# Performance work log

Hardware: AMD Instinct MI355X
Metric: run time of the kernel (lower is better)

Reference implementation:

```python
import jax, jax.numpy as jnp
import numpy as np

B, N, A, D = 16, 256, 64, 256


def setup_inputs() -> dict:
    key = jax.random.key(0)
    ks = jax.random.split(key, 9)
    s = 1.0 / np.sqrt(D)
    return {
        "cc_embeds": jax.random.normal(ks[0], (B, N, D), jnp.float32),
        "anchor_embeds": jax.random.normal(ks[1], (B, N, A, D), jnp.float32),
        "sims": jax.random.normal(ks[2], (B, N, A), jnp.float32),
        "Wq": jax.random.normal(ks[3], (D, D), jnp.float32) * s,
        "bq": jax.random.normal(ks[4], (D,), jnp.float32) * s,
        "Wk": jax.random.normal(ks[5], (D, D), jnp.float32) * s,
        "bk": jax.random.normal(ks[6], (D,), jnp.float32) * s,
        "Wv": jax.random.normal(ks[7], (D, D), jnp.float32) * s,
        "bv": jax.random.normal(ks[8], (D,), jnp.float32) * s,
    }


def reference(cc_embeds, anchor_embeds, sims, Wq, bq, Wk, bk, Wv, bv):
    # Linear projections (torch nn.Linear: x @ W.T + b)
    Q = cc_embeds @ Wq.T + bq                    # [B, N, D]
    K = anchor_embeds @ Wk.T + bk                # [B, N, A, D]
    V = anchor_embeds @ Wv.T + bv                # [B, N, A, D]
    scale = 1.0 / jnp.sqrt(jnp.asarray(D, Q.dtype))
    scores = jnp.einsum('bnd,bnad->bna', Q, K) * scale  # [B, N, A]
    adj = scores + sims                          # additive similarity bias
    # conditional softmax: rows whose raw sum == 0 are passed through unchanged
    nonzero = jnp.sum(adj, axis=-1, keepdims=True) != 0
    probs = jnp.where(nonzero, jax.nn.softmax(adj, axis=-1), adj)
    out = jnp.einsum('bna,bnad->bnd', probs, V)  # [B, N, D]
    return out[:, :, None, :]                    # match torch output [B, N, 1, D]
```

## Files before the change

kernel.cpp:

```cpp
#include <hip/hip_runtime.h>
#include <hip/hip_bf16.h>


__global__ __launch_bounds__(256) void k1_prep(
    const float* __restrict__ Wq, const float* __restrict__ bq,
    const float* __restrict__ Wk, const float* __restrict__ bk,
    const float* __restrict__ Wv,
    float* __restrict__ M, float* __restrict__ rvec, float* __restrict__ uvec,
    float* __restrict__ s0, float* __restrict__ WvT) {
  __shared__ float colL[256];
  __shared__ float pr[256];
  __shared__ float tile[64][65];
  const int tid = threadIdx.x;
  const int bid = blockIdx.x;
  if (bid < 256) {
    colL[tid] = Wq[tid * 256 + bid];
    __syncthreads();
    float acc = 0.f;
#pragma unroll 4
    for (int d = 0; d < 256; ++d) acc += colL[d] * Wk[d * 256 + tid];
    M[bid * 256 + tid] = acc;
  } else if (bid == 256) {
    colL[tid] = bq[tid];
    __syncthreads();
    float acc = 0.f;
#pragma unroll 4
    for (int d = 0; d < 256; ++d) acc += colL[d] * Wk[d * 256 + tid];
    rvec[tid] = acc;
  } else if (bid == 257) {
    colL[tid] = bk[tid];
    pr[tid] = bq[tid] * bk[tid];
    __syncthreads();
    float acc = 0.f;
#pragma unroll 4
    for (int d = 0; d < 256; ++d) acc += Wq[d * 256 + tid] * colL[d];
    uvec[tid] = acc;
    if (tid == 0) {
      float s = 0.f;
      for (int d = 0; d < 256; ++d) s += pr[d];
      s0[0] = s;
    }
  } else {
    const int tb = bid - 258, bi = tb >> 2, bj = tb & 3;
#pragma unroll
    for (int k = 0; k < 16; ++k) {
      int idx = k * 256 + tid;
      int r = idx >> 6, cL = idx & 63;
      tile[r][cL] = Wv[(bi * 64 + r) * 256 + bj * 64 + cL];
    }
    __syncthreads();
#pragma unroll
    for (int k = 0; k < 16; ++k) {
      int idx = k * 256 + tid;
      int r = idx >> 6, cL = idx & 63;
      WvT[(bj * 64 + r) * 256 + bi * 64 + cL] = tile[cL][r];
    }
  }
}

__global__ __launch_bounds__(256) void k2_proj(
    const float* __restrict__ cc, const float* __restrict__ M,
    const float* __restrict__ rvec, const float* __restrict__ uvec,
    const float* __restrict__ s0p,
    float* __restrict__ tmat, float* __restrict__ cvec) {
  __shared__ __align__(16) float ccT[256 * 8];
  __shared__ float uL[256];
  const int tid = threadIdx.x;
  const int i0 = blockIdx.x * 8;
  const float4* g4 = (const float4*)(cc + (size_t)i0 * 256);
#pragma unroll
  for (int k = 0; k < 2; ++k) {
    int f = k * 256 + tid;
    float4 v = g4[f];
    int row = f >> 6;
    int e = (f & 63) << 2;
    ccT[(e + 0) * 8 + row] = v.x;
    ccT[(e + 1) * 8 + row] = v.y;
    ccT[(e + 2) * 8 + row] = v.z;
    ccT[(e + 3) * 8 + row] = v.w;
  }
  uL[tid] = uvec[tid];
  __syncthreads();
  float acc[8] = {0.f, 0.f, 0.f, 0.f, 0.f, 0.f, 0.f, 0.f};
#pragma unroll 4
  for (int e = 0; e < 256; ++e) {
    float m = M[e * 256 + tid];
    const float4* cr = (const float4*)(ccT + e * 8);
    float4 c0 = cr[0], c1 = cr[1];
    acc[0] += c0.x * m; acc[1] += c0.y * m; acc[2] += c0.z * m; acc[3] += c0.w * m;
    acc[4] += c1.x * m; acc[5] += c1.y * m; acc[6] += c1.z * m; acc[7] += c1.w * m;
  }
  float rv = rvec[tid];
#pragma unroll
  for (int r = 0; r < 8; ++r) tmat[(size_t)(i0 + r) * 256 + tid] = acc[r] + rv;
  const int r = tid >> 5, j = tid & 31;
  float pc = 0.f;
#pragma unroll
  for (int k = 0; k < 8; ++k) pc += ccT[(j + 32 * k) * 8 + r] * uL[j + 32 * k];
  for (int off = 16; off >= 1; off >>= 1) pc += __shfl_xor(pc, off, 32);
  if (j == 0) cvec[i0 + r] = pc + s0p[0];
}

__global__ __launch_bounds__(256) void k3_attn(
    const float* __restrict__ anchor, const float* __restrict__ sims,
    const float* __restrict__ tmat, const float* __restrict__ cvec,
    float* __restrict__ wout, float* __restrict__ psum) {
  __shared__ float sL[64];
  __shared__ float pL[64];
  __shared__ __align__(16) float pW[4 * 256];
  __shared__ float psh;
  const int i = blockIdx.x;
  const int tid = threadIdx.x;
  const int lane = tid & 63, w = tid >> 6;

  const float4* g4 = (const float4*)(anchor + (size_t)i * 16384);
  float4 v[16];
#pragma unroll
  for (int k = 0; k < 16; ++k) v[k] = g4[k * 256 + tid];
  const float4 t4 = ((const float4*)(tmat + (size_t)i * 256))[lane];

#pragma unroll
  for (int k = 0; k < 16; ++k) {
    float s = v[k].x * t4.x + v[k].y * t4.y + v[k].z * t4.z + v[k].w * t4.w;
#pragma unroll
    for (int off = 32; off >= 1; off >>= 1) s += __shfl_xor(s, off, 64);
    if (lane == 0) sL[k * 4 + w] = s;
  }
  __syncthreads();
  if (tid < 64) {
    float adj = (sL[tid] + cvec[i]) * 0.0625f + sims[(size_t)i * 64 + tid];
    float ssum = adj, smax = adj;
    for (int off = 32; off >= 1; off >>= 1) {
      ssum += __shfl_xor(ssum, off, 64);
      smax = fmaxf(smax, __shfl_xor(smax, off, 64));
    }
    float p;
    if (ssum != 0.f) {
      p = expf(adj - smax);
      float z = p;
      for (int off = 32; off >= 1; off >>= 1) z += __shfl_xor(z, off, 64);
      p = p / z;
    } else {
      p = adj;
    }
    float ps = p;
    for (int off = 32; off >= 1; off >>= 1) ps += __shfl_xor(ps, off, 64);
    pL[tid] = p;
    if (tid == 0) psh = ps;
  }
  __syncthreads();
  float4 acc = {0.f, 0.f, 0.f, 0.f};
#pragma unroll
  for (int k = 0; k < 16; ++k) {
    float p = pL[k * 4 + w];
    acc.x += p * v[k].x; acc.y += p * v[k].y;
    acc.z += p * v[k].z; acc.w += p * v[k].w;
  }
  ((float4*)(pW + w * 256))[lane] = acc;
  __syncthreads();
  float val = pW[tid] + pW[256 + tid] + pW[512 + tid] + pW[768 + tid];
  wout[(size_t)i * 256 + tid] = val;
  if (tid == 0) psum[i] = psh;
}

__global__ __launch_bounds__(256) void k4_out(
    const float* __restrict__ wmat, const float* __restrict__ WvT,
    const float* __restrict__ bv, const float* __restrict__ psum,
    float* __restrict__ out) {
  __shared__ __align__(16) float wT[256 * 8];
  __shared__ float psL[8];
  const int tid = threadIdx.x;
  const int i0 = blockIdx.x * 8;
  const float4* g4 = (const float4*)(wmat + (size_t)i0 * 256);
#pragma unroll
  for (int k = 0; k < 2; ++k) {
    int f = k * 256 + tid;
    float4 v = g4[f];
    int row = f >> 6;
    int e = (f & 63) << 2;
    wT[(e + 0) * 8 + row] = v.x;
    wT[(e + 1) * 8 + row] = v.y;
    wT[(e + 2) * 8 + row] = v.z;
    wT[(e + 3) * 8 + row] = v.w;
  }
  if (tid < 8) psL[tid] = psum[i0 + tid];
  __syncthreads();
  float acc[8] = {0.f, 0.f, 0.f, 0.f, 0.f, 0.f, 0.f, 0.f};
#pragma unroll 4
  for (int e = 0; e < 256; ++e) {
    float m = WvT[e * 256 + tid];
    const float4* wr = (const float4*)(wT + e * 8);
    float4 c0 = wr[0], c1 = wr[1];
    acc[0] += c0.x * m; acc[1] += c0.y * m; acc[2] += c0.z * m; acc[3] += c0.w * m;
    acc[4] += c1.x * m; acc[5] += c1.y * m; acc[6] += c1.z * m; acc[7] += c1.w * m;
  }
  float b = bv[tid];
#pragma unroll
  for (int r = 0; r < 8; ++r)
    out[(size_t)(i0 + r) * 256 + tid] = acc[r] + b * psL[r];
}

extern "C" void kernel_launch(void* const* d_in, const int* in_sizes, int n_in,
                              void* d_out, int out_size, void* d_ws, size_t ws_size,
                              hipStream_t stream) {
  const float* cc     = (const float*)d_in[0];
  const float* anchor = (const float*)d_in[1];
  const float* sims   = (const float*)d_in[2];
  const float* Wq     = (const float*)d_in[3];
  const float* bq     = (const float*)d_in[4];
  const float* Wk     = (const float*)d_in[5];
  const float* bk     = (const float*)d_in[6];
  const float* Wv     = (const float*)d_in[7];
  const float* bv     = (const float*)d_in[8];
  float* out = (float*)d_out;
  float* ws  = (float*)d_ws;

  float* M    = ws;
  float* WvT  = ws + 65536;
  float* rvec = ws + 131072;
  float* uvec = ws + 131328;
  float* s0   = ws + 131584;
  float* cvec = ws + 131840;
  float* psum = ws + 135936;
  float* tmat = ws + 140032;
  float* wmat = tmat + 1048576;

  k1_prep<<<274, 256, 0, stream>>>(Wq, bq, Wk, bk, Wv, M, rvec, uvec, s0, WvT);
  k2_proj<<<512, 256, 0, stream>>>(cc, M, rvec, uvec, s0, tmat, cvec);
  k3_attn<<<4096, 256, 0, stream>>>(anchor, sims, tmat, cvec, wmat, psum);
  k4_out<<<512, 256, 0, stream>>>(wmat, WvT, bv, psum, out);
}
```

Measured before the change: 461.0 us.

## Split-K projection GEMVs with readlane broadcast and nontemporal anchor loads

The small projection kernels (k2 and k4) now split the reduction dimension across the four wavefronts. Each lane holds one input element per row and broadcasts it with readlane, and each lane computes four output columns using vector loads of the weight matrix. The partial sums are combined through shared memory. The attention kernel loads the streamed anchor tensor with nontemporal loads so it does not pollute the cache. The cost is more shared memory and registers in the GEMV kernels, while the dominant streaming kernel is left mostly unchanged.

```diff
diff --git a/kernel.cpp b/kernel.cpp
--- a/kernel.cpp
+++ b/kernel.cpp
@@ -1,6 +1,12 @@
 #include <hip/hip_runtime.h>
 #include <hip/hip_bf16.h>
 
+
+typedef float f4 __attribute__((ext_vector_type(4)));
+
+__device__ __forceinline__ float bcast_lane(float x, int lane) {
+  return __int_as_float(__builtin_amdgcn_readlane(__float_as_int(x), lane));
+}
 
 __global__ __launch_bounds__(256) void k1_prep(
     const float* __restrict__ Wq, const float* __restrict__ bq,
@@ -63,42 +69,45 @@
     const float* __restrict__ rvec, const float* __restrict__ uvec,
     const float* __restrict__ s0p,
     float* __restrict__ tmat, float* __restrict__ cvec) {
-  __shared__ __align__(16) float ccT[256 * 8];
-  __shared__ float uL[256];
-  const int tid = threadIdx.x;
+  __shared__ __align__(16) float pOut[4][8][256];
+  __shared__ float cpart[4][8];
+  const int tid = threadIdx.x;
+  const int w = tid >> 6, L = tid & 63;
   const int i0 = blockIdx.x * 8;
-  const float4* g4 = (const float4*)(cc + (size_t)i0 * 256);
-#pragma unroll
-  for (int k = 0; k < 2; ++k) {
-    int f = k * 256 + tid;
-    float4 v = g4[f];
-    int row = f >> 6;
-    int e = (f & 63) << 2;
-    ccT[(e + 0) * 8 + row] = v.x;
-    ccT[(e + 1) * 8 + row] = v.y;
-    ccT[(e + 2) * 8 + row] = v.z;
-    ccT[(e + 3) * 8 + row] = v.w;
-  }
-  uL[tid] = uvec[tid];
-  __syncthreads();
-  float acc[8] = {0.f, 0.f, 0.f, 0.f, 0.f, 0.f, 0.f, 0.f};
-#pragma unroll 4
-  for (int e = 0; e < 256; ++e) {
-    float m = M[e * 256 + tid];
-    const float4* cr = (const float4*)(ccT + e * 8);
-    float4 c0 = cr[0], c1 = cr[1];
-    acc[0] += c0.x * m; acc[1] += c0.y * m; acc[2] += c0.z * m; acc[3] += c0.w * m;
-    acc[4] += c1.x * m; acc[5] += c1.y * m; acc[6] += c1.z * m; acc[7] += c1.w * m;
-  }
+  const int e0 = w * 64;
+  float ccreg[8];
+#pragma unroll
+  for (int r = 0; r < 8; ++r) ccreg[r] = cc[(size_t)(i0 + r) * 256 + e0 + L];
+  float uvl = uvec[e0 + L];
+  f4 acc[8] = {};
+#pragma unroll 8
+  for (int ee = 0; ee < 64; ++ee) {
+    f4 m = *(const f4*)(M + (size_t)(e0 + ee) * 256 + 4 * L);
+#pragma unroll
+    for (int r = 0; r < 8; ++r) {
+      float cv = bcast_lane(ccreg[r], ee);
+      acc[r].x += cv * m.x; acc[r].y += cv * m.y;
+      acc[r].z += cv * m.z; acc[r].w += cv * m.w;
+    }
+  }
+#pragma unroll
+  for (int r = 0; r < 8; ++r) *(f4*)&pOut[w][r][4 * L] = acc[r];
+#pragma unroll
+  for (int r = 0; r < 8; ++r) {
+    float pc = ccreg[r] * uvl;
+#pragma unroll
+    for (int off = 32; off >= 1; off >>= 1) pc += __shfl_xor(pc, off, 64);
+    if (L == 0) cpart[w][r] = pc;
+  }
+  __syncthreads();
   float rv = rvec[tid];
 #pragma unroll
-  for (int r = 0; r < 8; ++r) tmat[(size_t)(i0 + r) * 256 + tid] = acc[r] + rv;
-  const int r = tid >> 5, j = tid & 31;
-  float pc = 0.f;
-#pragma unroll
-  for (int k = 0; k < 8; ++k) pc += ccT[(j + 32 * k) * 8 + r] * uL[j + 32 * k];
-  for (int off = 16; off >= 1; off >>= 1) pc += __shfl_xor(pc, off, 32);
-  if (j == 0) cvec[i0 + r] = pc + s0p[0];
+  for (int r = 0; r < 8; ++r) {
+    float s = pOut[0][r][tid] + pOut[1][r][tid] + pOut[2][r][tid] + pOut[3][r][tid];
+    tmat[(size_t)(i0 + r) * 256 + tid] = s + rv;
+  }
+  if (tid < 8)
+    cvec[i0 + tid] = cpart[0][tid] + cpart[1][tid] + cpart[2][tid] + cpart[3][tid] + s0p[0];
 }
 
 __global__ __launch_bounds__(256) void k3_attn(
@@ -113,11 +122,11 @@
   const int tid = threadIdx.x;
   const int lane = tid & 63, w = tid >> 6;
 
-  const float4* g4 = (const float4*)(anchor + (size_t)i * 16384);
-  float4 v[16];
-#pragma unroll
-  for (int k = 0; k < 16; ++k) v[k] = g4[k * 256 + tid];
-  const float4 t4 = ((const float4*)(tmat + (size_t)i * 256))[lane];
+  const f4* g4 = (const f4*)(anchor + (size_t)i * 16384);
+  f4 v[16];
+#pragma unroll
+  for (int k = 0; k < 16; ++k) v[k] = __builtin_nontemporal_load(g4 + k * 256 + tid);
+  const f4 t4 = ((const f4*)(tmat + (size_t)i * 256))[lane];
 
 #pragma unroll
   for (int k = 0; k < 16; ++k) {
@@ -149,14 +158,14 @@
     if (tid == 0) psh = ps;
   }
   __syncthreads();
-  float4 acc = {0.f, 0.f, 0.f, 0.f};
+  f4 acc = {0.f, 0.f, 0.f, 0.f};
 #pragma unroll
   for (int k = 0; k < 16; ++k) {
     float p = pL[k * 4 + w];
     acc.x += p * v[k].x; acc.y += p * v[k].y;
     acc.z += p * v[k].z; acc.w += p * v[k].w;
   }
-  ((float4*)(pW + w * 256))[lane] = acc;
+  *(f4*)(pW + w * 256 + 4 * lane) = acc;
   __syncthreads();
   float val = pW[tid] + pW[256 + tid] + pW[512 + tid] + pW[768 + tid];
   wout[(size_t)i * 256 + tid] = val;
@@ -167,37 +176,34 @@
     const float* __restrict__ wmat, const float* __restrict__ WvT,
     const float* __restrict__ bv, const float* __restrict__ psum,
     float* __restrict__ out) {
-  __shared__ __align__(16) float wT[256 * 8];
-  __shared__ float psL[8];
-  const int tid = threadIdx.x;
+  __shared__ __align__(16) float pOut[4][8][256];
+  const int tid = threadIdx.x;
+  const int w = tid >> 6, L = tid & 63;
   const int i0 = blockIdx.x * 8;
-  const float4* g4 = (const float4*)(wmat + (size_t)i0 * 256);
-#pragma unroll
-  for (int k = 0; k < 2; ++k) {
-    int f = k * 256 + tid;
-    float4 v = g4[f];
-    int row = f >> 6;
-    int e = (f & 63) << 2;
-    wT[(e + 0) * 8 + row] = v.x;
-    wT[(e + 1) * 8 + row] = v.y;
-    wT[(e + 2) * 8 + row] = v.z;
-    wT[(e + 3) * 8 + row] = v.w;
-  }
-  if (tid < 8) psL[tid] = psum[i0 + tid];
-  __syncthreads();
-  float acc[8] = {0.f, 0.f, 0.f, 0.f, 0.f, 0.f, 0.f, 0.f};
-#pragma unroll 4
-  for (int e = 0; e < 256; ++e) {
-    float m = WvT[e * 256 + tid];
-    const float4* wr = (const float4*)(wT + e * 8);
-    float4 c0 = wr[0], c1 = wr[1];
-    acc[0] += c0.x * m; acc[1] += c0.y * m; acc[2] += c0.z * m; acc[3] += c0.w * m;
-    acc[4] += c1.x * m; acc[5] += c1.y * m; acc[6] += c1.z * m; acc[7] += c1.w * m;
-  }
+  const int e0 = w * 64;
+  float wreg[8];
+#pragma unroll
+  for (int r = 0; r < 8; ++r) wreg[r] = wmat[(size_t)(i0 + r) * 256 + e0 + L];
+  f4 acc[8] = {};
+#pragma unroll 8
+  for (int ee = 0; ee < 64; ++ee) {
+    f4 m = *(const f4*)(WvT + (size_t)(e0 + ee) * 256 + 4 * L);
+#pragma unroll
+    for (int r = 0; r < 8; ++r) {
+      float cv = bcast_lane(wreg[r], ee);
+      acc[r].x += cv * m.x; acc[r].y += cv * m.y;
+      acc[r].z += cv * m.z; acc[r].w += cv * m.w;
+    }
+  }
+#pragma unroll
+  for (int r = 0; r < 8; ++r) *(f4*)&pOut[w][r][4 * L] = acc[r];
+  __syncthreads();
   float b = bv[tid];
 #pragma unroll
-  for (int r = 0; r < 8; ++r)
-    out[(size_t)(i0 + r) * 256 + tid] = acc[r] + b * psL[r];
+  for (int r = 0; r < 8; ++r) {
+    float s = pOut[0][r][tid] + pOut[1][r][tid] + pOut[2][r][tid] + pOut[3][r][tid];
+    out[(size_t)(i0 + r) * 256 + tid] = s + b * psum[i0 + r];
+  }
 }
 
 extern "C" void kernel_launch(void* const* d_in, const int* in_sizes, int n_in,
```

New measurement: 414.6 us. 1.11x faster.
